# Kernel tuning notes

Measured on AMD Instinct MI355X. Metric: run time of the kernel, lower is better.

Reference implementation:

```python
import jax, jax.numpy as jnp
import numpy as np

B, T, ND, DH, DZ = 32, 4096, 32, 128, 128
IN_DIM = 2 * ND + DH  # 192


def setup_inputs() -> dict:
    key = jax.random.key(0)
    ks = jax.random.split(key, 11)
    s = 1.0 / np.sqrt(DZ)  # PyTorch GRUCell init scale
    return {
        "z0": jax.random.normal(ks[0], (B, DZ), jnp.float32),
        # sorted irregular timestamps per series
        "t_dyn": jnp.sort(jax.random.uniform(ks[1], (B, T), jnp.float32) * 100.0, axis=1),
        "Y_dyn": jax.random.normal(ks[2], (B, T, ND), jnp.float32),
        "M_dyn": (jax.random.uniform(ks[3], (B, T, ND)) > 0.5).astype(jnp.float32),
        "dyn_lens": jax.random.randint(ks[4], (B,), 1, T + 1, dtype=jnp.int32),
        "h_path_vals": jax.random.normal(ks[5], (B, T, DH), jnp.float32),
        "W_ih": jax.random.uniform(ks[6], (3 * DZ, IN_DIM), jnp.float32, -s, s),
        "b_ih": jax.random.uniform(ks[7], (3 * DZ,), jnp.float32, -s, s),
        "W_hh": jax.random.uniform(ks[8], (3 * DZ, DZ), jnp.float32, -s, s),
        "b_hh": jax.random.uniform(ks[9], (3 * DZ,), jnp.float32, -s, s),
        "log_gamma": jnp.zeros((DZ,), jnp.float32),
    }


def reference(z0, t_dyn, Y_dyn, M_dyn, dyn_lens, h_path_vals, W_ih, b_ih, W_hh, b_hh, log_gamma):
    gamma = jax.nn.softplus(log_gamma)  # (d_z,)
    Tm = t_dyn.shape[1]
    # concat dynamic features once; precompute all input-side gate projections as one big GEMM
    x = jnp.concatenate([Y_dyn, M_dyn, h_path_vals], axis=-1)        # (B,T,IN_DIM)
    gi_all = jnp.einsum('bti,gi->btg', x, W_ih) + b_ih               # (B,T,3*d_z)
    active = (jnp.arange(Tm)[:, None] < dyn_lens[None, :]).astype(z0.dtype)  # (T,B)

    def step(carry, xs):
        z, t_prev = carry
        t_k, gi, a = xs                 # (B,), (B,3dz), (B,)
        dt = jnp.maximum(t_k - t_prev, 0.0)
        z_d = z * jnp.exp(-gamma * dt[:, None])      # exponential decay
        gh = z_d @ W_hh.T + b_hh
        i_r, i_u, i_n = jnp.split(gi, 3, axis=-1)
        h_r, h_u, h_n = jnp.split(gh, 3, axis=-1)
        r = jax.nn.sigmoid(i_r + h_r)
        u = jax.nn.sigmoid(i_u + h_u)
        n = jnp.tanh(i_n + r * h_n)
        z_new = (1.0 - u) * n + u * z_d
        am = a[:, None]
        z_out = am * z_new + (1.0 - am) * z_d        # length masking
        return (z_out, t_k), z_out

    xs = (t_dyn.T, jnp.swapaxes(gi_all, 0, 1), active)  # time-major
    (z_final, _), Z = jax.lax.scan(step, (z0, t_dyn[:, 0]), xs)
    Z_traj = jnp.swapaxes(Z, 0, 1)                      # (B,T,d_z)
    return z_final, Z_traj
```

## Files before the change

kernel.cpp:

```cpp
#include <hip/hip_runtime.h>
#include <hip/hip_bf16.h>
#include <stdint.h>

typedef unsigned short u16;

#define NB  32
#define NT  4096
#define NDZ 128
#define NG  384
#define NIN 192

__device__ __forceinline__ float rlane(float v, int k) {
  return __int_as_float(__builtin_amdgcn_readlane(__float_as_int(v), k));
}
__device__ __forceinline__ float fast_rcp(float x) { return __builtin_amdgcn_rcpf(x); }
__device__ __forceinline__ float sigmoid_f(float x) { return fast_rcp(1.f + __expf(-x)); }
__device__ __forceinline__ float tanh_f(float x) {
  return 1.f - 2.f * fast_rcp(1.f + __expf(2.f * x));
}
__device__ __forceinline__ u16 f2bf(float f) {
  unsigned u = __float_as_uint(f);
  return (u16)((u + 0x7fffu + ((u >> 16) & 1u)) >> 16);
}
__device__ __forceinline__ float bf2f(u16 u) { return __uint_as_float((unsigned)u << 16); }

__device__ __forceinline__ void bar_lds() {
  asm volatile("s_waitcnt lgkmcnt(0)\n\ts_barrier" ::: "memory");
}

__device__ __forceinline__ float giload(const float* p) { return *p; }
__device__ __forceinline__ float giload(const u16* p)   { return bf2f(*p); }
__device__ __forceinline__ void store8(float* p, const float* v) {
  float4 a = {v[0], v[1], v[2], v[3]}, b = {v[4], v[5], v[6], v[7]};
  *(float4*)p = a; *(float4*)(p + 4) = b;
}
__device__ __forceinline__ void store8(u16* p, const float* v) {
  uint4 o;
  o.x = (unsigned)f2bf(v[0]) | ((unsigned)f2bf(v[1]) << 16);
  o.y = (unsigned)f2bf(v[2]) | ((unsigned)f2bf(v[3]) << 16);
  o.z = (unsigned)f2bf(v[4]) | ((unsigned)f2bf(v[5]) << 16);
  o.w = (unsigned)f2bf(v[6]) | ((unsigned)f2bf(v[7]) << 16);
  *(uint4*)p = o;
}

#define GM 128
#define GN 128
#define LDSS 132

template <typename GT>
__global__ __launch_bounds__(256) void gemm_gi(
    const float* __restrict__ Y, const float* __restrict__ M,
    const float* __restrict__ H, const float* __restrict__ Wih,
    const float* __restrict__ bih, GT* __restrict__ gi)
{
  __shared__ float As[32 * LDSS];
  __shared__ float Bs[32 * LDSS];
  const int tid = threadIdx.x;
  const size_t m0 = (size_t)blockIdx.x * GM;
  const int n0 = blockIdx.y * GN;
  const int tm = tid & 15;
  const int tn = tid >> 4;

  float acc[8][8];
#pragma unroll
  for (int i = 0; i < 8; ++i)
#pragma unroll
    for (int j = 0; j < 8; ++j) acc[i][j] = 0.f;

#pragma unroll
  for (int kc = 0; kc < 6; ++kc) {
    const float* src; int stride; int off;
    if (kc == 0)      { src = Y; stride = 32;  off = 0; }
    else if (kc == 1) { src = M; stride = 32;  off = 0; }
    else              { src = H; stride = 128; off = (kc - 2) * 32; }
#pragma unroll
    for (int it = 0; it < 4; ++it) {
      int x = tid + it * 256;
      int row = x >> 3, q = x & 7;
      float4 v = *(const float4*)(src + (m0 + (size_t)row) * stride + off + q * 4);
      As[(q * 4 + 0) * LDSS + row] = v.x;
      As[(q * 4 + 1) * LDSS + row] = v.y;
      As[(q * 4 + 2) * LDSS + row] = v.z;
      As[(q * 4 + 3) * LDSS + row] = v.w;
    }
#pragma unroll
    for (int it = 0; it < 4; ++it) {
      int x = tid + it * 256;
      int g = x >> 3, q = x & 7;
      float4 v = *(const float4*)(Wih + (size_t)(n0 + g) * NIN + kc * 32 + q * 4);
      Bs[(q * 4 + 0) * LDSS + g] = v.x;
      Bs[(q * 4 + 1) * LDSS + g] = v.y;
      Bs[(q * 4 + 2) * LDSS + g] = v.z;
      Bs[(q * 4 + 3) * LDSS + g] = v.w;
    }
    __syncthreads();
#pragma unroll
    for (int kk = 0; kk < 32; ++kk) {
      float4 a0 = *(const float4*)&As[kk * LDSS + tm * 8];
      float4 a1 = *(const float4*)&As[kk * LDSS + tm * 8 + 4];
      float4 b0 = *(const float4*)&Bs[kk * LDSS + tn * 8];
      float4 b1 = *(const float4*)&Bs[kk * LDSS + tn * 8 + 4];
      float av[8] = {a0.x, a0.y, a0.z, a0.w, a1.x, a1.y, a1.z, a1.w};
      float bv[8] = {b0.x, b0.y, b0.z, b0.w, b1.x, b1.y, b1.z, b1.w};
#pragma unroll
      for (int i = 0; i < 8; ++i)
#pragma unroll
        for (int j = 0; j < 8; ++j)
          acc[i][j] = __builtin_fmaf(av[i], bv[j], acc[i][j]);
    }
    __syncthreads();
  }
  float bv[8];
#pragma unroll
  for (int j = 0; j < 8; ++j) bv[j] = bih[n0 + tn * 8 + j];
#pragma unroll
  for (int i = 0; i < 8; ++i) {
    size_t row = m0 + (size_t)(tm * 8 + i);
    GT* o = gi + row * NG + n0 + tn * 8;
    float v[8];
#pragma unroll
    for (int j = 0; j < 8; ++j) v[j] = acc[i][j] + bv[j];
    store8(o, v);
  }
}

#define KS 32

template <typename GT>
__global__ __launch_bounds__(512, 2) void scan_k(
    const float* __restrict__ zinit, const float* __restrict__ tdyn,
    const int* __restrict__ lens, const float* __restrict__ Whh,
    const float* __restrict__ bhh, const float* __restrict__ lgam,
    const GT* __restrict__ gi, float* __restrict__ out)
{
  const int b = blockIdx.x;
  const int tid = threadIdx.x;
  const int lane = tid & 63;
  const int w = tid >> 6;
  const int s_idx = w & 3;
  const int h = w >> 2;
  const int k0 = s_idx * KS;
  const int e = lane & 31;
  const int hi = lane >> 5;
  const int j = k0 + e;

  __shared__ float P0[4][NG];
  __shared__ float P1[4][NG];

  const int rowA = h * NDZ + lane;
  const int rowB = rowA + 64;
  const int rowC = 2 * NDZ + h * 64 + lane;
  float wa[KS], wb[KS], wc[KS];
  {
    const float4* ra = (const float4*)(Whh + (size_t)rowA * NDZ + k0);
    const float4* rb = (const float4*)(Whh + (size_t)rowB * NDZ + k0);
    const float4* rc = (const float4*)(Whh + (size_t)rowC * NDZ + k0);
#pragma unroll
    for (int q = 0; q < 8; ++q) {
      float4 va = ra[q], vb = rb[q], vc = rc[q];
      wa[4 * q + 0] = va.x; wa[4 * q + 1] = va.y; wa[4 * q + 2] = va.z; wa[4 * q + 3] = va.w;
      wb[4 * q + 0] = vb.x; wb[4 * q + 1] = vb.y; wb[4 * q + 2] = vb.z; wb[4 * q + 3] = vb.w;
      wc[4 * q + 0] = vc.x; wc[4 * q + 1] = vc.y; wc[4 * q + 2] = vc.z; wc[4 * q + 3] = vc.w;
    }
  }

  const int len = lens[b];
  const float* tp = tdyn + (size_t)b * NT;
  const GT* gb = gi + (size_t)b * NT * NG;
  float* traj = out + (size_t)NB * NDZ + (size_t)b * NT * NDZ;

  float zc = zinit[b * NDZ + j];
  const float lg = lgam[j];
  const float gam = (lg > 15.f) ? lg : __logf(1.f + __expf(lg));
  const float br = bhh[j], bu = bhh[NDZ + j], bn = bhh[2 * NDZ + j];
  float t_prev = tp[0];
  float zdr = zc;

  const int prow = hi ? (NDZ + j) : j;
  const int nrow = 2 * NDZ + j;
  const int nq = hi * 2;

  float ptkA = tp[1];
  float ptkB = tp[2];
  float pgrA = giload(gb + j), pguA = giload(gb + NDZ + j), pgnA = giload(gb + 2 * NDZ + j);
  float pgrB = giload(gb + NG + j), pguB = giload(gb + NG + NDZ + j), pgnB = giload(gb + NG + 2 * NDZ + j);

  auto stepf = [&](float (*PB)[NG], float& ptkX, float& pgrX, float& pguX, float& pgnX, int t) {
    const float tk = ptkX;
    const float ef = __expf(-gam * fmaxf(tk - t_prev, 0.f));
    t_prev = tk;

    const bool active = (t < len);
    if (active) {
      float aa = 0.f, ab = 0.f, ac = 0.f;
#pragma unroll
      for (int k = 0; k < KS; ++k) {
        const float zk = rlane(zdr, k);
        aa = __builtin_fmaf(wa[k], zk, aa);
        ab = __builtin_fmaf(wb[k], zk, ab);
        ac = __builtin_fmaf(wc[k], zk, ac);
      }
      PB[s_idx][rowA] = aa;
      PB[s_idx][rowB] = ab;
      PB[s_idx][rowC] = ac;
    }
    bar_lds();

    const float zd = zdr;
    if (active) {
      const float p0 = PB[0][prow], p1 = PB[1][prow];
      const float p2 = PB[2][prow], p3 = PB[3][prow];
      const float n0 = PB[nq][nrow], n1 = PB[nq + 1][nrow];
      const float prim = (p0 + p1) + (p2 + p3);
      const float n2 = n0 + n1;
      const float oth = __shfl(prim, lane ^ 32, 64);
      const float nx  = __shfl(n2,   lane ^ 32, 64);
      const float snv = n2 + nx;
      const float sr = hi ? oth  : prim;
      const float su = hi ? prim : oth;
      const float cr = br + pgrX, cu = bu + pguX, cn = bn;
      const float r = sigmoid_f(sr + cr);
      const float u = sigmoid_f(su + cu);
      const float n = tanh_f(__builtin_fmaf(r, snv + cn, pgnX));
      zc = (1.f - u) * n + u * zd;
    } else {
      zc = zd;
    }
    if (h == 0 && lane < 32) traj[(size_t)t * NDZ + j] = zc;

    zdr = zc * ef;

    const int t2 = (t + 2 < NT) ? (t + 2) : (NT - 1);
    const int t3 = (t + 3 < NT) ? (t + 3) : (NT - 1);
    ptkX = tp[t3];
    const GT* g2 = gb + (size_t)t2 * NG;
    pgrX = giload(g2 + j);
    pguX = giload(g2 + NDZ + j);
    pgnX = giload(g2 + 2 * NDZ + j);
  };

  for (int t = 0; t < NT; t += 2) {
    stepf(P0, ptkA, pgrA, pguA, pgnA, t);
    stepf(P1, ptkB, pgrB, pguB, pgnB, t + 1);
  }
  if (h == 0 && lane < 32) out[b * NDZ + j] = zc;
}

extern "C" void kernel_launch(void* const* d_in, const int* in_sizes, int n_in,
                              void* d_out, int out_size, void* d_ws, size_t ws_size,
                              hipStream_t stream) {
  const float* z0   = (const float*)d_in[0];
  const float* tdyn = (const float*)d_in[1];
  const float* Y    = (const float*)d_in[2];
  const float* M    = (const float*)d_in[3];
  const int*   lens = (const int*)d_in[4];
  const float* H    = (const float*)d_in[5];
  const float* Wih  = (const float*)d_in[6];
  const float* bih  = (const float*)d_in[7];
  const float* Whh  = (const float*)d_in[8];
  const float* bhh  = (const float*)d_in[9];
  const float* lgam = (const float*)d_in[10];
  float* out = (float*)d_out;

  const size_t needF32 = (size_t)NB * NT * NG * sizeof(float);
  dim3 ggrid((NB * NT) / GM, NG / GN);
  if (ws_size >= needF32) {
    float* gi = (float*)d_ws;
    gemm_gi<float><<<ggrid, 256, 0, stream>>>(Y, M, H, Wih, bih, gi);
    scan_k<float><<<dim3(NB), 512, 0, stream>>>(z0, tdyn, lens, Whh, bhh, lgam, gi, out);
  } else {
    u16* gi = (u16*)d_ws;
    gemm_gi<u16><<<ggrid, 256, 0, stream>>>(Y, M, H, Wih, bih, gi);
    scan_k<u16><<<dim3(NB), 512, 0, stream>>>(z0, tdyn, lens, Whh, bhh, lgam, gi, out);
  }
}
```

Measured before the change: 3.548 ms.

## Use packed fp16 dot2 for recurrent matvec and simplify gate reduction

Stores the W_hh slices in registers as packed half2 and computes the per-step recurrent matvec with v_dot2 instructions. Lanes pack their z value together with their neighbour's, so only half as many readlanes are needed. The gate reduction now has every lane read all 12 partial sums from LDS directly, replacing the split by lane half plus cross-half shuffles. This halves weight register use and the number of FMA instructions, but weights and the hidden state are rounded to fp16 every step, which may hurt accuracy over the 4096-step recurrence.

```diff
diff --git a/kernel.cpp b/kernel.cpp
--- a/kernel.cpp
+++ b/kernel.cpp
@@ -3,6 +3,7 @@
 #include <stdint.h>
 
 typedef unsigned short u16;
+typedef __fp16 h2 __attribute__((ext_vector_type(2)));
 
 #define NB  32
 #define NT  4096
@@ -10,9 +11,12 @@
 #define NG  384
 #define NIN 192
 
-__device__ __forceinline__ float rlane(float v, int k) {
-  return __int_as_float(__builtin_amdgcn_readlane(__float_as_int(v), k));
-}
+#if defined(__has_builtin)
+#if __has_builtin(__builtin_amdgcn_fdot2)
+#define HAS_FDOT2 1
+#endif
+#endif
+
 __device__ __forceinline__ float fast_rcp(float x) { return __builtin_amdgcn_rcpf(x); }
 __device__ __forceinline__ float sigmoid_f(float x) { return fast_rcp(1.f + __expf(-x)); }
 __device__ __forceinline__ float tanh_f(float x) {
@@ -141,7 +145,6 @@
   const int h = w >> 2;
   const int k0 = s_idx * KS;
   const int e = lane & 31;
-  const int hi = lane >> 5;
   const int j = k0 + e;
 
   __shared__ float P0[4][NG];
@@ -150,6 +153,24 @@
   const int rowA = h * NDZ + lane;
   const int rowB = rowA + 64;
   const int rowC = 2 * NDZ + h * 64 + lane;
+#ifdef HAS_FDOT2
+  h2 wa[KS / 2], wb[KS / 2], wc[KS / 2];
+  {
+    const float4* ra = (const float4*)(Whh + (size_t)rowA * NDZ + k0);
+    const float4* rb = (const float4*)(Whh + (size_t)rowB * NDZ + k0);
+    const float4* rc = (const float4*)(Whh + (size_t)rowC * NDZ + k0);
+#pragma unroll
+    for (int q = 0; q < 8; ++q) {
+      float4 va = ra[q], vb = rb[q], vc = rc[q];
+      wa[2 * q]     = __builtin_amdgcn_cvt_pkrtz(va.x, va.y);
+      wa[2 * q + 1] = __builtin_amdgcn_cvt_pkrtz(va.z, va.w);
+      wb[2 * q]     = __builtin_amdgcn_cvt_pkrtz(vb.x, vb.y);
+      wb[2 * q + 1] = __builtin_amdgcn_cvt_pkrtz(vb.z, vb.w);
+      wc[2 * q]     = __builtin_amdgcn_cvt_pkrtz(vc.x, vc.y);
+      wc[2 * q + 1] = __builtin_amdgcn_cvt_pkrtz(vc.z, vc.w);
+    }
+  }
+#else
   float wa[KS], wb[KS], wc[KS];
   {
     const float4* ra = (const float4*)(Whh + (size_t)rowA * NDZ + k0);
@@ -158,11 +179,12 @@
 #pragma unroll
     for (int q = 0; q < 8; ++q) {
       float4 va = ra[q], vb = rb[q], vc = rc[q];
-      wa[4 * q + 0] = va.x; wa[4 * q + 1] = va.y; wa[4 * q + 2] = va.z; wa[4 * q + 3] = va.w;
-      wb[4 * q + 0] = vb.x; wb[4 * q + 1] = vb.y; wb[4 * q + 2] = vb.z; wb[4 * q + 3] = vb.w;
-      wc[4 * q + 0] = vc.x; wc[4 * q + 1] = vc.y; wc[4 * q + 2] = vc.z; wc[4 * q + 3] = vc.w;
-    }
-  }
+      wa[4 * q] = va.x; wa[4 * q + 1] = va.y; wa[4 * q + 2] = va.z; wa[4 * q + 3] = va.w;
+      wb[4 * q] = vb.x; wb[4 * q + 1] = vb.y; wb[4 * q + 2] = vb.z; wb[4 * q + 3] = vb.w;
+      wc[4 * q] = vc.x; wc[4 * q + 1] = vc.y; wc[4 * q + 2] = vc.z; wc[4 * q + 3] = vc.w;
+    }
+  }
+#endif
 
   const int len = lens[b];
   const float* tp = tdyn + (size_t)b * NT;
@@ -176,10 +198,6 @@
   float t_prev = tp[0];
   float zdr = zc;
 
-  const int prow = hi ? (NDZ + j) : j;
-  const int nrow = 2 * NDZ + j;
-  const int nq = hi * 2;
-
   float ptkA = tp[1];
   float ptkB = tp[2];
   float pgrA = giload(gb + j), pguA = giload(gb + NDZ + j), pgnA = giload(gb + 2 * NDZ + j);
@@ -193,13 +211,28 @@
     const bool active = (t < len);
     if (active) {
       float aa = 0.f, ab = 0.f, ac = 0.f;
+#ifdef HAS_FDOT2
+      const float zpartner = __shfl_xor(zdr, 1, 64);
+      const h2 zpk = __builtin_amdgcn_cvt_pkrtz(zdr, zpartner);
+      const int zpi = __builtin_bit_cast(int, zpk);
+#pragma unroll
+      for (int m = 0; m < KS / 2; ++m) {
+        const int zi = __builtin_amdgcn_readlane(zpi, 2 * m);
+        const h2 zk = __builtin_bit_cast(h2, zi);
+        aa = __builtin_amdgcn_fdot2(wa[m], zk, aa, false);
+        ab = __builtin_amdgcn_fdot2(wb[m], zk, ab, false);
+        ac = __builtin_amdgcn_fdot2(wc[m], zk, ac, false);
+      }
+#else
 #pragma unroll
       for (int k = 0; k < KS; ++k) {
-        const float zk = rlane(zdr, k);
+        const float zk = __int_as_float(
+            __builtin_amdgcn_readlane(__float_as_int(zdr), k));
         aa = __builtin_fmaf(wa[k], zk, aa);
         ab = __builtin_fmaf(wb[k], zk, ab);
         ac = __builtin_fmaf(wc[k], zk, ac);
       }
+#endif
       PB[s_idx][rowA] = aa;
       PB[s_idx][rowB] = ab;
       PB[s_idx][rowC] = ac;
@@ -208,20 +241,15 @@
 
     const float zd = zdr;
     if (active) {
-      const float p0 = PB[0][prow], p1 = PB[1][prow];
-      const float p2 = PB[2][prow], p3 = PB[3][prow];
-      const float n0 = PB[nq][nrow], n1 = PB[nq + 1][nrow];
-      const float prim = (p0 + p1) + (p2 + p3);
-      const float n2 = n0 + n1;
-      const float oth = __shfl(prim, lane ^ 32, 64);
-      const float nx  = __shfl(n2,   lane ^ 32, 64);
-      const float snv = n2 + nx;
-      const float sr = hi ? oth  : prim;
-      const float su = hi ? prim : oth;
-      const float cr = br + pgrX, cu = bu + pguX, cn = bn;
-      const float r = sigmoid_f(sr + cr);
-      const float u = sigmoid_f(su + cu);
-      const float n = tanh_f(__builtin_fmaf(r, snv + cn, pgnX));
+      const float* Pb = &PB[0][0];
+      const float sr = (Pb[j] + Pb[NG + j]) + (Pb[2 * NG + j] + Pb[3 * NG + j]);
+      const float su = (Pb[NDZ + j] + Pb[NG + NDZ + j]) +
+                       (Pb[2 * NG + NDZ + j] + Pb[3 * NG + NDZ + j]);
+      const float sn = (Pb[2 * NDZ + j] + Pb[NG + 2 * NDZ + j]) +
+                       (Pb[2 * NG + 2 * NDZ + j] + Pb[3 * NG + 2 * NDZ + j]);
+      const float r = sigmoid_f(sr + br + pgrX);
+      const float u = sigmoid_f(su + bu + pguX);
+      const float n = tanh_f(__builtin_fmaf(r, sn + bn, pgnX));
       zc = (1.f - u) * n + u * zd;
     } else {
       zc = zd;
```

Measured after the change: 2.941 ms. 1.21x faster.
